# Optimization experiments

Hardware: AMD Instinct MI355X
Metric: run time of the kernel (lower is better)

The kernel has to match this reference:

```python
import jax, jax.numpy as jnp
import numpy as np

M = 0.25
S = 64.0  # gamma
OP = 1.0 + M      # optimum for positives
ON = -M           # optimum for negatives
DELTA_P = 1.0 - M
DELTA_N = M
EPS = 1e-12       # F.normalize eps

B, D, C = 256, 512, 100000


def setup_inputs() -> dict:
    key = jax.random.key(0)
    k1, k2, k3, k4 = jax.random.split(key, 4)
    x = jax.random.normal(k1, (B, D), dtype=jnp.float32)
    emb = jax.random.normal(k2, (B, D), dtype=jnp.float32)
    W = jax.random.normal(k3, (C, D), dtype=jnp.float32) * 0.02  # fc.weight [C, D]
    labels = jax.random.randint(k4, (B,), 0, C, dtype=jnp.int64)
    return {"x": x, "labels": labels, "emb": emb, "W": W}


def reference(x, labels, emb, W):
    # x is unused in the original forward (dead argument)
    # F.normalize(emb): L2-normalize rows with eps clamp
    norm = jnp.linalg.norm(emb, axis=1, keepdims=True)
    ff = emb / jnp.maximum(norm, EPS)
    # fc(ff): linear classifier (weights NOT normalized; the torch loop is a no-op)
    wf = ff @ W.T  # [B, C]
    wf_d = jax.lax.stop_gradient(wf)

    rows = jnp.arange(wf.shape[0])
    sp_logit = wf[rows, labels]        # torch.diagonal(wf.T[labels])
    sp_logit_d = wf_d[rows, labels]

    alpha_p = jnp.maximum(OP - sp_logit_d, 0.0)          # clamp_min(-s_p + Op, 0)
    sp = jnp.exp(-S * alpha_p * (sp_logit - DELTA_P))    # [B]

    # negatives: all classes except the label column (mask instead of cat-slicing)
    neg_mask = jnp.asarray(rows[:, None] >= 0, wf.dtype) * (1.0 - jax.nn.one_hot(labels, wf.shape[1], dtype=wf.dtype))
    alpha_n = jnp.maximum(wf_d + M, 0.0)                 # clamp_min(s_n - On, 0)
    sn = jnp.exp(S * alpha_n * (wf - DELTA_N)) * neg_mask  # label column zeroed out

    loss = jnp.log(1.0 + sn.sum() * sp.sum())
    return loss
```

## Files before the change

### kernel.cpp

```cpp
#include <hip/hip_runtime.h>
#include <hip/hip_bf16.h>

typedef __attribute__((ext_vector_type(8))) __bf16 bf16x8;
typedef __attribute__((ext_vector_type(4))) float f32x4;

#define B_M 256
#define K_D 512
#define N_C 100000
#define BN 64
#define BK 64
#define NBLK ((N_C + BN - 1) / BN)

__device__ __forceinline__ unsigned short f2bf(float x) {
  unsigned int u = __float_as_uint(x);
  u += 0x7fffu + ((u >> 16) & 1u);
  return (unsigned short)(u >> 16);
}

__global__ __launch_bounds__(256) void norm_kernel(const float* __restrict__ emb,
                                                   unsigned short* __restrict__ ff) {
  const int row = blockIdx.x;
  const int t = threadIdx.x;
  float a = emb[row * K_D + t];
  float b = emb[row * K_D + t + 256];
  float ss = a * a + b * b;
  #pragma unroll
  for (int o = 32; o > 0; o >>= 1) ss += __shfl_down(ss, o, 64);
  __shared__ float red[4];
  const int wid = t >> 6, lane = t & 63;
  if (lane == 0) red[wid] = ss;
  __syncthreads();
  float tot = red[0] + red[1] + red[2] + red[3];
  float rn = 1.0f / fmaxf(sqrtf(tot), 1e-12f);
  ff[row * K_D + t]       = f2bf(a * rn);
  ff[row * K_D + t + 256] = f2bf(b * rn);
}

__global__ __launch_bounds__(512) void gemm_loss_kernel(const unsigned short* __restrict__ ff,
                                                        const float* __restrict__ W,
                                                        const int* __restrict__ labels,
                                                        double* __restrict__ partials) {
  __shared__ __align__(16) unsigned short As[B_M * BK];
  __shared__ __align__(16) unsigned short Bs[BN * BK];
  __shared__ int lbl[B_M];
  __shared__ double red[16];

  const int tid = threadIdx.x;
  const int wid = tid >> 6;
  const int lane = tid & 63;
  const int n0 = blockIdx.x * BN;

  if (tid < B_M) lbl[tid] = labels[tid];

  f32x4 acc[2][4] = {};

  const int wrow = wid * 32;
  const int l15 = lane & 15;
  const int lhi = lane >> 4;

  const int bcol = tid >> 3;
  const int bk8  = tid & 7;
  const long long jrow = (long long)n0 + bcol;

  for (int kk = 0; kk < K_D / BK; ++kk) {
    if (kk) __syncthreads();
    #pragma unroll
    for (int it = 0; it < 4; ++it) {
      int idx = it * 512 + tid;
      int row = idx >> 3;
      int kc  = idx & 7;
      uint4 v = *reinterpret_cast<const uint4*>(ff + row * K_D + kk * BK + kc * 8);
      int off = (row * 128 + kc * 16) ^ ((row & 7) << 4);
      *reinterpret_cast<uint4*>(reinterpret_cast<char*>(As) + off) = v;
    }
    {
      float4 f0 = {0.f, 0.f, 0.f, 0.f}, f1 = {0.f, 0.f, 0.f, 0.f};
      if (jrow < N_C) {
        const float* gp = W + jrow * K_D + kk * BK + bk8 * 8;
        f0 = *reinterpret_cast<const float4*>(gp);
        f1 = *reinterpret_cast<const float4*>(gp + 4);
      }
      union { unsigned short us[8]; uint4 v; } pk;
      pk.us[0] = f2bf(f0.x); pk.us[1] = f2bf(f0.y); pk.us[2] = f2bf(f0.z); pk.us[3] = f2bf(f0.w);
      pk.us[4] = f2bf(f1.x); pk.us[5] = f2bf(f1.y); pk.us[6] = f2bf(f1.z); pk.us[7] = f2bf(f1.w);
      int off = (bcol * 128 + bk8 * 16) ^ ((bcol & 7) << 4);
      *reinterpret_cast<uint4*>(reinterpret_cast<char*>(Bs) + off) = pk.v;
    }
    __syncthreads();

    bf16x8 afr[2][2], bfr[4][2];
    #pragma unroll
    for (int fm = 0; fm < 2; ++fm)
      #pragma unroll
      for (int ks = 0; ks < 2; ++ks) {
        int row = wrow + fm * 16 + l15;
        int off = (row * 128 + ks * 64 + lhi * 16) ^ ((row & 7) << 4);
        afr[fm][ks] = *reinterpret_cast<const bf16x8*>(reinterpret_cast<const char*>(As) + off);
      }
    #pragma unroll
    for (int fn = 0; fn < 4; ++fn)
      #pragma unroll
      for (int ks = 0; ks < 2; ++ks) {
        int col = fn * 16 + l15;
        int off = (col * 128 + ks * 64 + lhi * 16) ^ ((col & 7) << 4);
        bfr[fn][ks] = *reinterpret_cast<const bf16x8*>(reinterpret_cast<const char*>(Bs) + off);
      }
    #pragma unroll
    for (int fm = 0; fm < 2; ++fm)
      #pragma unroll
      for (int fn = 0; fn < 4; ++fn)
        #pragma unroll
        for (int ks = 0; ks < 2; ++ks)
          acc[fm][fn] = __builtin_amdgcn_mfma_f32_16x16x32_bf16(afr[fm][ks], bfr[fn][ks], acc[fm][fn], 0, 0, 0);
  }

  float sn_local = 0.0f;
  double sp_local = 0.0;
  #pragma unroll
  for (int fm = 0; fm < 2; ++fm)
    #pragma unroll
    for (int fn = 0; fn < 4; ++fn)
      #pragma unroll
      for (int r = 0; r < 4; ++r) {
        int row = wrow + fm * 16 + lhi * 4 + r;
        int j = n0 + fn * 16 + l15;
        float v = acc[fm][fn][r];
        if (j < N_C) {
          if (j == lbl[row]) {
            double alpha = fmax(1.25 - (double)v, 0.0);
            sp_local += exp(-64.0 * alpha * ((double)v - 0.75));
          } else {
            float an = fmaxf(v + 0.25f, 0.0f);
            sn_local += __expf(64.0f * an * (v - 0.25f));
          }
        }
      }

  double sn_d = (double)sn_local;
  #pragma unroll
  for (int o = 32; o > 0; o >>= 1) {
    sn_d     += __shfl_down(sn_d, o, 64);
    sp_local += __shfl_down(sp_local, o, 64);
  }
  if (lane == 0) { red[wid] = sn_d; red[8 + wid] = sp_local; }
  __syncthreads();
  if (tid == 0) {
    double a = 0.0, b = 0.0;
    #pragma unroll
    for (int i = 0; i < 8; ++i) { a += red[i]; b += red[8 + i]; }
    partials[blockIdx.x] = a;
    partials[NBLK + blockIdx.x] = b;
  }
}

__global__ __launch_bounds__(512) void finalize_kernel(const double* __restrict__ partials,
                                                       float* __restrict__ out) {
  const int t = threadIdx.x;
  double sn = 0.0, sp = 0.0;
  for (int i = t; i < NBLK; i += 512) { sn += partials[i]; sp += partials[NBLK + i]; }
  #pragma unroll
  for (int o = 32; o > 0; o >>= 1) { sn += __shfl_down(sn, o, 64); sp += __shfl_down(sp, o, 64); }
  __shared__ double red[16];
  const int wid = t >> 6, lane = t & 63;
  if (lane == 0) { red[wid] = sn; red[8 + wid] = sp; }
  __syncthreads();
  if (t == 0) {
    double a = 0.0, b = 0.0;
    for (int i = 0; i < 8; ++i) { a += red[i]; b += red[8 + i]; }
    out[0] = (float)log1p(a * b);
  }
}

extern "C" void kernel_launch(void* const* d_in, const int* in_sizes, int n_in,
                              void* d_out, int out_size, void* d_ws, size_t ws_size,
                              hipStream_t stream) {
  const int*   labels = (const int*)d_in[1];
  const float* emb    = (const float*)d_in[2];
  const float* W      = (const float*)d_in[3];
  float* out = (float*)d_out;

  unsigned short* ff = (unsigned short*)d_ws;
  double* partials = (double*)((char*)d_ws + (size_t)B_M * K_D * 2);

  norm_kernel<<<B_M, 256, 0, stream>>>(emb, ff);
  gemm_loss_kernel<<<NBLK, 512, 0, stream>>>(ff, W, labels, partials);
  finalize_kernel<<<1, 512, 0, stream>>>(partials, out);
}
```

Baseline: 73.61 us.

## Pipeline W loads with register prefetch and double-buffered LDS, load A directly

Drops the shared-memory staging of the normalized activations and has each wave load its A fragments straight from global memory, prefetching the next k-step. W tiles are prefetched three steps ahead into registers and written into a double-buffered LDS tile, so there is a single barrier per k-step. This is meant to hide global-load latency behind the MFMA work and cut LDS traffic and barrier count. In exchange it raises register pressure and moves the A traffic onto uncoalesced per-lane global (L2-cached) reads.

```diff
diff --git a/kernel.cpp b/kernel.cpp
--- a/kernel.cpp
+++ b/kernel.cpp
@@ -8,13 +8,20 @@
 #define K_D 512
 #define N_C 100000
 #define BN 64
-#define BK 64
+#define BKS 64
+#define NSTEP (K_D / BKS)
 #define NBLK ((N_C + BN - 1) / BN)
 
 __device__ __forceinline__ unsigned short f2bf(float x) {
   unsigned int u = __float_as_uint(x);
   u += 0x7fffu + ((u >> 16) & 1u);
   return (unsigned short)(u >> 16);
+}
+
+__device__ __forceinline__ void block_sync() {
+  asm volatile("s_waitcnt lgkmcnt(0)" ::: "memory");
+  __builtin_amdgcn_s_barrier();
+  __builtin_amdgcn_sched_barrier(0);
 }
 
 __global__ __launch_bounds__(256) void norm_kernel(const float* __restrict__ emb,
@@ -40,91 +47,105 @@
                                                         const float* __restrict__ W,
                                                         const int* __restrict__ labels,
                                                         double* __restrict__ partials) {
-  __shared__ __align__(16) unsigned short As[B_M * BK];
-  __shared__ __align__(16) unsigned short Bs[BN * BK];
+  __shared__ __align__(16) unsigned short Bs[2][BN * BKS];
   __shared__ int lbl[B_M];
   __shared__ double red[16];
 
   const int tid = threadIdx.x;
   const int wid = tid >> 6;
   const int lane = tid & 63;
-  const int n0 = blockIdx.x * BN;
-
-  if (tid < B_M) lbl[tid] = labels[tid];
-
-  f32x4 acc[2][4] = {};
-
-  const int wrow = wid * 32;
   const int l15 = lane & 15;
   const int lhi = lane >> 4;
+  const int n0 = blockIdx.x * BN;
+
+  if (tid < B_M) lbl[tid] = labels[tid];
 
   const int bcol = tid >> 3;
   const int bk8  = tid & 7;
-  const long long jrow = (long long)n0 + bcol;
-
-  for (int kk = 0; kk < K_D / BK; ++kk) {
-    if (kk) __syncthreads();
-    #pragma unroll
-    for (int it = 0; it < 4; ++it) {
-      int idx = it * 512 + tid;
-      int row = idx >> 3;
-      int kc  = idx & 7;
-      uint4 v = *reinterpret_cast<const uint4*>(ff + row * K_D + kk * BK + kc * 8);
-      int off = (row * 128 + kc * 16) ^ ((row & 7) << 4);
-      *reinterpret_cast<uint4*>(reinterpret_cast<char*>(As) + off) = v;
-    }
-    {
-      float4 f0 = {0.f, 0.f, 0.f, 0.f}, f1 = {0.f, 0.f, 0.f, 0.f};
-      if (jrow < N_C) {
-        const float* gp = W + jrow * K_D + kk * BK + bk8 * 8;
-        f0 = *reinterpret_cast<const float4*>(gp);
-        f1 = *reinterpret_cast<const float4*>(gp + 4);
-      }
-      union { unsigned short us[8]; uint4 v; } pk;
-      pk.us[0] = f2bf(f0.x); pk.us[1] = f2bf(f0.y); pk.us[2] = f2bf(f0.z); pk.us[3] = f2bf(f0.w);
-      pk.us[4] = f2bf(f1.x); pk.us[5] = f2bf(f1.y); pk.us[6] = f2bf(f1.z); pk.us[7] = f2bf(f1.w);
-      int off = (bcol * 128 + bk8 * 16) ^ ((bcol & 7) << 4);
-      *reinterpret_cast<uint4*>(reinterpret_cast<char*>(Bs) + off) = pk.v;
-    }
-    __syncthreads();
-
-    bf16x8 afr[2][2], bfr[4][2];
-    #pragma unroll
-    for (int fm = 0; fm < 2; ++fm)
-      #pragma unroll
-      for (int ks = 0; ks < 2; ++ks) {
-        int row = wrow + fm * 16 + l15;
-        int off = (row * 128 + ks * 64 + lhi * 16) ^ ((row & 7) << 4);
-        afr[fm][ks] = *reinterpret_cast<const bf16x8*>(reinterpret_cast<const char*>(As) + off);
-      }
-    #pragma unroll
-    for (int fn = 0; fn < 4; ++fn)
-      #pragma unroll
-      for (int ks = 0; ks < 2; ++ks) {
-        int col = fn * 16 + l15;
-        int off = (col * 128 + ks * 64 + lhi * 16) ^ ((col & 7) << 4);
-        bfr[fn][ks] = *reinterpret_cast<const bf16x8*>(reinterpret_cast<const char*>(Bs) + off);
-      }
-    #pragma unroll
-    for (int fm = 0; fm < 2; ++fm)
-      #pragma unroll
-      for (int fn = 0; fn < 4; ++fn)
+  const bool valid = (n0 + bcol) < N_C;
+  const float* wp = W + (long long)(n0 + bcol) * K_D + bk8 * 8;
+  const int woff = (bcol * 128 + bk8 * 16) ^ ((bcol & 7) << 4);
+
+  const unsigned short* ap = ff + (wid * 32 + l15) * K_D + lhi * 8;
+
+  f32x4 acc[2][4] = {};
+  float4 wf0[3], wf1[3];
+  bf16x8 acur[2][2], anxt[2][2];
+
+  #pragma unroll
+  for (int mt = 0; mt < 2; ++mt)
+    #pragma unroll
+    for (int ks = 0; ks < 2; ++ks)
+      acur[mt][ks] = *reinterpret_cast<const bf16x8*>(ap + mt * 16 * K_D + ks * 32);
+
+  #pragma unroll
+  for (int s = 0; s < 3; ++s) {
+    if (valid) {
+      wf0[s] = *reinterpret_cast<const float4*>(wp + s * BKS);
+      wf1[s] = *reinterpret_cast<const float4*>(wp + s * BKS + 4);
+    } else {
+      wf0[s] = float4{0.f, 0.f, 0.f, 0.f};
+      wf1[s] = float4{0.f, 0.f, 0.f, 0.f};
+    }
+  }
+  {
+    union { unsigned short us[8]; uint4 v; } pk;
+    pk.us[0] = f2bf(wf0[0].x); pk.us[1] = f2bf(wf0[0].y); pk.us[2] = f2bf(wf0[0].z); pk.us[3] = f2bf(wf0[0].w);
+    pk.us[4] = f2bf(wf1[0].x); pk.us[5] = f2bf(wf1[0].y); pk.us[6] = f2bf(wf1[0].z); pk.us[7] = f2bf(wf1[0].w);
+    *reinterpret_cast<uint4*>(reinterpret_cast<char*>(&Bs[0][0]) + woff) = pk.v;
+  }
+  block_sync();
+
+  #pragma unroll
+  for (int t = 0; t < NSTEP; ++t) {
+    const int cb = t & 1;
+    if (t + 3 < NSTEP && valid) {
+      wf0[t % 3] = *reinterpret_cast<const float4*>(wp + (t + 3) * BKS);
+      wf1[t % 3] = *reinterpret_cast<const float4*>(wp + (t + 3) * BKS + 4);
+    }
+    if (t + 1 < NSTEP) {
+      #pragma unroll
+      for (int mt = 0; mt < 2; ++mt)
         #pragma unroll
         for (int ks = 0; ks < 2; ++ks)
-          acc[fm][fn] = __builtin_amdgcn_mfma_f32_16x16x32_bf16(afr[fm][ks], bfr[fn][ks], acc[fm][fn], 0, 0, 0);
+          anxt[mt][ks] = *reinterpret_cast<const bf16x8*>(ap + mt * 16 * K_D + (t + 1) * BKS + ks * 32);
+      const int s = (t + 1) % 3;
+      union { unsigned short us[8]; uint4 v; } pk;
+      pk.us[0] = f2bf(wf0[s].x); pk.us[1] = f2bf(wf0[s].y); pk.us[2] = f2bf(wf0[s].z); pk.us[3] = f2bf(wf0[s].w);
+      pk.us[4] = f2bf(wf1[s].x); pk.us[5] = f2bf(wf1[s].y); pk.us[6] = f2bf(wf1[s].z); pk.us[7] = f2bf(wf1[s].w);
+      *reinterpret_cast<uint4*>(reinterpret_cast<char*>(&Bs[cb ^ 1][0]) + woff) = pk.v;
+    }
+    #pragma unroll
+    for (int fn = 0; fn < 4; ++fn) {
+      #pragma unroll
+      for (int ks = 0; ks < 2; ++ks) {
+        const int col = fn * 16 + l15;
+        const int boff = (col * 128 + ks * 64 + lhi * 16) ^ ((col & 7) << 4);
+        bf16x8 b = *reinterpret_cast<const bf16x8*>(reinterpret_cast<const char*>(&Bs[cb][0]) + boff);
+        #pragma unroll
+        for (int mt = 0; mt < 2; ++mt)
+          acc[mt][fn] = __builtin_amdgcn_mfma_f32_16x16x32_bf16(acur[mt][ks], b, acc[mt][fn], 0, 0, 0);
+      }
+    }
+    block_sync();
+    #pragma unroll
+    for (int mt = 0; mt < 2; ++mt)
+      #pragma unroll
+      for (int ks = 0; ks < 2; ++ks)
+        acur[mt][ks] = anxt[mt][ks];
   }
 
   float sn_local = 0.0f;
   double sp_local = 0.0;
   #pragma unroll
-  for (int fm = 0; fm < 2; ++fm)
+  for (int mt = 0; mt < 2; ++mt)
     #pragma unroll
     for (int fn = 0; fn < 4; ++fn)
       #pragma unroll
       for (int r = 0; r < 4; ++r) {
-        int row = wrow + fm * 16 + lhi * 4 + r;
+        int row = wid * 32 + mt * 16 + lhi * 4 + r;
         int j = n0 + fn * 16 + l15;
-        float v = acc[fm][fn][r];
+        float v = acc[mt][fn][r];
         if (j < N_C) {
           if (j == lbl[row]) {
             double alpha = fmax(1.25 - (double)v, 0.0);
```

Result: slower. 80.93 us (+10.0%).

## Double-buffer ff tile via direct global-to-LDS loads and register-prefetch W fragments

Applied to the files above, without the earlier changes.

Restructures the GEMM main loop. The ff tile is double-buffered in LDS using global_load_lds with an XOR swizzle. W is no longer staged through LDS: each wave reads its 16 W columns straight into registers, prefetched two K-steps ahead, and converts them to bf16 in place. The warp layout changes to 2x4 so each wave computes 128 rows by 16 columns. The goal is to overlap global loads with MFMA work and remove the W shared-memory round trip, at the cost of hand-written waitcnt and sched_barrier sequencing that is fragile and adds register pressure.

```diff
diff --git a/kernel.cpp b/kernel.cpp
--- a/kernel.cpp
+++ b/kernel.cpp
@@ -9,12 +9,28 @@
 #define N_C 100000
 #define BN 64
 #define BK 64
+#define NSTEP (K_D / BK)
 #define NBLK ((N_C + BN - 1) / BN)
+
+#define SB() __builtin_amdgcn_sched_barrier(0)
 
 __device__ __forceinline__ unsigned short f2bf(float x) {
   unsigned int u = __float_as_uint(x);
   u += 0x7fffu + ((u >> 16) & 1u);
   return (unsigned short)(u >> 16);
+}
+
+__device__ __forceinline__ bf16x8 pack8(float4 a, float4 b) {
+  union { unsigned short us[8]; bf16x8 v; } u;
+  u.us[0] = f2bf(a.x); u.us[1] = f2bf(a.y); u.us[2] = f2bf(a.z); u.us[3] = f2bf(a.w);
+  u.us[4] = f2bf(b.x); u.us[5] = f2bf(b.y); u.us[6] = f2bf(b.z); u.us[7] = f2bf(b.w);
+  return u.v;
+}
+
+__device__ __forceinline__ void glds16(const void* g, void* l) {
+  __builtin_amdgcn_global_load_lds(
+      (const __attribute__((address_space(1))) unsigned int*)g,
+      (__attribute__((address_space(3))) unsigned int*)l, 16, 0, 0);
 }
 
 __global__ __launch_bounds__(256) void norm_kernel(const float* __restrict__ emb,
@@ -40,101 +56,118 @@
                                                         const float* __restrict__ W,
                                                         const int* __restrict__ labels,
                                                         double* __restrict__ partials) {
-  __shared__ __align__(16) unsigned short As[B_M * BK];
-  __shared__ __align__(16) unsigned short Bs[BN * BK];
+  __shared__ __align__(16) unsigned short As[2][B_M * BK];
   __shared__ int lbl[B_M];
   __shared__ double red[16];
 
   const int tid = threadIdx.x;
   const int wid = tid >> 6;
   const int lane = tid & 63;
-  const int n0 = blockIdx.x * BN;
-
-  if (tid < B_M) lbl[tid] = labels[tid];
-
-  f32x4 acc[2][4] = {};
-
-  const int wrow = wid * 32;
   const int l15 = lane & 15;
   const int lhi = lane >> 4;
-
-  const int bcol = tid >> 3;
-  const int bk8  = tid & 7;
-  const long long jrow = (long long)n0 + bcol;
-
-  for (int kk = 0; kk < K_D / BK; ++kk) {
-    if (kk) __syncthreads();
-    #pragma unroll
-    for (int it = 0; it < 4; ++it) {
-      int idx = it * 512 + tid;
-      int row = idx >> 3;
-      int kc  = idx & 7;
-      uint4 v = *reinterpret_cast<const uint4*>(ff + row * K_D + kk * BK + kc * 8);
-      int off = (row * 128 + kc * 16) ^ ((row & 7) << 4);
-      *reinterpret_cast<uint4*>(reinterpret_cast<char*>(As) + off) = v;
-    }
+  const int wm = wid & 1;
+  const int wn = wid >> 1;
+  const int n0 = blockIdx.x * BN;
+
+  if (tid < B_M) lbl[tid] = labels[tid];
+  SB();
+
+  const int jreal = n0 + wn * 16 + l15;
+  const int jcol = jreal < N_C ? jreal : (N_C - 1);
+  const float* wp = W + (long long)jcol * K_D + lhi * 8;
+
+  const int ao0 = l15 * 128 + ((0 * 64 + lhi * 16) ^ ((l15 & 7) << 4));
+  const int ao1 = l15 * 128 + ((1 * 64 + lhi * 16) ^ ((l15 & 7) << 4));
+
+  f32x4 acc[8] = {};
+  float4 wbuf[2][4];
+  bf16x8 bfr[2];
+
+  #pragma unroll
+  for (int it = 0; it < 4; ++it) {
+    int s = it * 512 + tid;
+    int row = s >> 3;
+    int k8 = (s & 7) ^ (row & 7);
+    glds16(ff + row * K_D + 0 * BK + k8 * 8, &As[0][0] + s * 8);
+  }
+  SB();
+  #pragma unroll
+  for (int st = 0; st < 2; ++st) {
+    wbuf[st][0] = *reinterpret_cast<const float4*>(wp + st * BK);
+    wbuf[st][1] = *reinterpret_cast<const float4*>(wp + st * BK + 4);
+    wbuf[st][2] = *reinterpret_cast<const float4*>(wp + st * BK + 32);
+    wbuf[st][3] = *reinterpret_cast<const float4*>(wp + st * BK + 36);
+  }
+  SB();
+  asm volatile("s_waitcnt vmcnt(8)" ::: "memory");
+  asm volatile("s_waitcnt lgkmcnt(0)" ::: "memory");
+  __builtin_amdgcn_s_barrier();
+  SB();
+
+  #pragma unroll
+  for (int t = 0; t < NSTEP; ++t) {
+    if (t + 1 < NSTEP) {
+      #pragma unroll
+      for (int it = 0; it < 4; ++it) {
+        int s = it * 512 + tid;
+        int row = s >> 3;
+        int k8 = (s & 7) ^ (row & 7);
+        glds16(ff + row * K_D + (t + 1) * BK + k8 * 8, &As[(t + 1) & 1][0] + s * 8);
+      }
+    }
+    SB();
+    if (t == 0) {
+      bfr[0] = pack8(wbuf[0][0], wbuf[0][1]);
+      bfr[1] = pack8(wbuf[0][2], wbuf[0][3]);
+      SB();
+    }
+    if (t + 2 < NSTEP) {
+      wbuf[t & 1][0] = *reinterpret_cast<const float4*>(wp + (t + 2) * BK);
+      wbuf[t & 1][1] = *reinterpret_cast<const float4*>(wp + (t + 2) * BK + 4);
+      wbuf[t & 1][2] = *reinterpret_cast<const float4*>(wp + (t + 2) * BK + 32);
+      wbuf[t & 1][3] = *reinterpret_cast<const float4*>(wp + (t + 2) * BK + 36);
+    }
+    SB();
     {
-      float4 f0 = {0.f, 0.f, 0.f, 0.f}, f1 = {0.f, 0.f, 0.f, 0.f};
-      if (jrow < N_C) {
-        const float* gp = W + jrow * K_D + kk * BK + bk8 * 8;
-        f0 = *reinterpret_cast<const float4*>(gp);
-        f1 = *reinterpret_cast<const float4*>(gp + 4);
+      const char* ab = reinterpret_cast<const char*>(&As[t & 1][0]);
+      #pragma unroll
+      for (int mf = 0; mf < 8; ++mf) {
+        const int base = (wm * 8 + mf) * 2048;
+        bf16x8 a0 = *reinterpret_cast<const bf16x8*>(ab + base + ao0);
+        bf16x8 a1 = *reinterpret_cast<const bf16x8*>(ab + base + ao1);
+        acc[mf] = __builtin_amdgcn_mfma_f32_16x16x32_bf16(a0, bfr[0], acc[mf], 0, 0, 0);
+        acc[mf] = __builtin_amdgcn_mfma_f32_16x16x32_bf16(a1, bfr[1], acc[mf], 0, 0, 0);
       }
-      union { unsigned short us[8]; uint4 v; } pk;
-      pk.us[0] = f2bf(f0.x); pk.us[1] = f2bf(f0.y); pk.us[2] = f2bf(f0.z); pk.us[3] = f2bf(f0.w);
-      pk.us[4] = f2bf(f1.x); pk.us[5] = f2bf(f1.y); pk.us[6] = f2bf(f1.z); pk.us[7] = f2bf(f1.w);
-      int off = (bcol * 128 + bk8 * 16) ^ ((bcol & 7) << 4);
-      *reinterpret_cast<uint4*>(reinterpret_cast<char*>(Bs) + off) = pk.v;
-    }
-    __syncthreads();
-
-    bf16x8 afr[2][2], bfr[4][2];
-    #pragma unroll
-    for (int fm = 0; fm < 2; ++fm)
-      #pragma unroll
-      for (int ks = 0; ks < 2; ++ks) {
-        int row = wrow + fm * 16 + l15;
-        int off = (row * 128 + ks * 64 + lhi * 16) ^ ((row & 7) << 4);
-        afr[fm][ks] = *reinterpret_cast<const bf16x8*>(reinterpret_cast<const char*>(As) + off);
-      }
-    #pragma unroll
-    for (int fn = 0; fn < 4; ++fn)
-      #pragma unroll
-      for (int ks = 0; ks < 2; ++ks) {
-        int col = fn * 16 + l15;
-        int off = (col * 128 + ks * 64 + lhi * 16) ^ ((col & 7) << 4);
-        bfr[fn][ks] = *reinterpret_cast<const bf16x8*>(reinterpret_cast<const char*>(Bs) + off);
-      }
-    #pragma unroll
-    for (int fm = 0; fm < 2; ++fm)
-      #pragma unroll
-      for (int fn = 0; fn < 4; ++fn)
-        #pragma unroll
-        for (int ks = 0; ks < 2; ++ks)
-          acc[fm][fn] = __builtin_amdgcn_mfma_f32_16x16x32_bf16(afr[fm][ks], bfr[fn][ks], acc[fm][fn], 0, 0, 0);
+    }
+    if (t + 1 < NSTEP) {
+      if (t + 2 < NSTEP) { asm volatile("s_waitcnt vmcnt(4)" ::: "memory"); }
+      else               { asm volatile("s_waitcnt vmcnt(0)" ::: "memory"); }
+      bfr[0] = pack8(wbuf[(t + 1) & 1][0], wbuf[(t + 1) & 1][1]);
+      bfr[1] = pack8(wbuf[(t + 1) & 1][2], wbuf[(t + 1) & 1][3]);
+      asm volatile("s_waitcnt lgkmcnt(0)" ::: "memory");
+      __builtin_amdgcn_s_barrier();
+      SB();
+    }
   }
 
   float sn_local = 0.0f;
   double sp_local = 0.0;
-  #pragma unroll
-  for (int fm = 0; fm < 2; ++fm)
+  if (jreal < N_C) {
     #pragma unroll
-    for (int fn = 0; fn < 4; ++fn)
+    for (int mf = 0; mf < 8; ++mf)
       #pragma unroll
       for (int r = 0; r < 4; ++r) {
-        int row = wrow + fm * 16 + lhi * 4 + r;
-        int j = n0 + fn * 16 + l15;
-        float v = acc[fm][fn][r];
-        if (j < N_C) {
-          if (j == lbl[row]) {
-            double alpha = fmax(1.25 - (double)v, 0.0);
-            sp_local += exp(-64.0 * alpha * ((double)v - 0.75));
-          } else {
-            float an = fmaxf(v + 0.25f, 0.0f);
-            sn_local += __expf(64.0f * an * (v - 0.25f));
-          }
+        int row = wm * 128 + mf * 16 + lhi * 4 + r;
+        float v = acc[mf][r];
+        if (jreal == lbl[row]) {
+          double alpha = fmax(1.25 - (double)v, 0.0);
+          sp_local += exp(-64.0 * alpha * ((double)v - 0.75));
+        } else {
+          float an = fmaxf(v + 0.25f, 0.0f);
+          sn_local += __expf(64.0f * an * (v - 0.25f));
         }
       }
+  }
 
   double sn_d = (double)sn_local;
   #pragma unroll
```

Measured after the change: 92.58 us. 25.8% more time.

## Replace LDS-staged GEMM with per-wave 64x64 register tiles loaded from global

Applied to the files above, without the earlier changes.

The shared-memory staging of A and B tiles and its barriers are removed. Each wave now computes an independent 64x64 output tile, loading bf16 A fragments and f32 W fragments directly from global memory into MFMA registers. This removes LDS traffic and synchronization. In exchange, each W tile is fetched and converted by four waves instead of once, and the global loads are strided per lane rather than coalesced.

```diff
diff --git a/kernel.cpp b/kernel.cpp
--- a/kernel.cpp
+++ b/kernel.cpp
@@ -7,14 +7,23 @@
 #define B_M 256
 #define K_D 512
 #define N_C 100000
-#define BN 64
-#define BK 64
-#define NBLK ((N_C + BN - 1) / BN)
+#define TM 64
+#define TN 64
+#define NT_N ((N_C + TN - 1) / TN)
+#define N_TILES (4 * NT_N)
+#define NBLK2 ((N_TILES + 7) / 8)
 
 __device__ __forceinline__ unsigned short f2bf(float x) {
   unsigned int u = __float_as_uint(x);
   u += 0x7fffu + ((u >> 16) & 1u);
   return (unsigned short)(u >> 16);
+}
+
+__device__ __forceinline__ bf16x8 pack8(float4 a, float4 b) {
+  union { unsigned short us[8]; bf16x8 v; } u;
+  u.us[0] = f2bf(a.x); u.us[1] = f2bf(a.y); u.us[2] = f2bf(a.z); u.us[3] = f2bf(a.w);
+  u.us[4] = f2bf(b.x); u.us[5] = f2bf(b.y); u.us[6] = f2bf(b.z); u.us[7] = f2bf(b.w);
+  return u.v;
 }
 
 __global__ __launch_bounds__(256) void norm_kernel(const float* __restrict__ emb,
@@ -40,93 +49,73 @@
                                                         const float* __restrict__ W,
                                                         const int* __restrict__ labels,
                                                         double* __restrict__ partials) {
-  __shared__ __align__(16) unsigned short As[B_M * BK];
-  __shared__ __align__(16) unsigned short Bs[BN * BK];
   __shared__ int lbl[B_M];
   __shared__ double red[16];
 
   const int tid = threadIdx.x;
   const int wid = tid >> 6;
   const int lane = tid & 63;
-  const int n0 = blockIdx.x * BN;
-
-  if (tid < B_M) lbl[tid] = labels[tid];
-
-  f32x4 acc[2][4] = {};
-
-  const int wrow = wid * 32;
   const int l15 = lane & 15;
   const int lhi = lane >> 4;
 
-  const int bcol = tid >> 3;
-  const int bk8  = tid & 7;
-  const long long jrow = (long long)n0 + bcol;
+  if (tid < B_M) lbl[tid] = labels[tid];
+  __syncthreads();
 
-  for (int kk = 0; kk < K_D / BK; ++kk) {
-    if (kk) __syncthreads();
+  const int tile = blockIdx.x * 8 + wid;
+  const bool live = tile < N_TILES;
+  const int mt = (tile & 3) * TM;
+  const int nt = (tile >> 2) * TN;
+
+  const unsigned short* apf[4];
+  const float* wpf[4];
+  bool cvalid[4];
+  #pragma unroll
+  for (int i = 0; i < 4; ++i) {
+    int arow = mt + i * 16 + l15;
+    apf[i] = ff + arow * K_D + lhi * 8;
+    int col = nt + i * 16 + l15;
+    cvalid[i] = live && (col < N_C);
+    int cc = (col < N_C && live) ? col : 0;
+    wpf[i] = W + (long long)cc * K_D + lhi * 8;
+  }
+
+  f32x4 acc[4][4] = {};
+
+  if (live) {
     #pragma unroll
-    for (int it = 0; it < 4; ++it) {
-      int idx = it * 512 + tid;
-      int row = idx >> 3;
-      int kc  = idx & 7;
-      uint4 v = *reinterpret_cast<const uint4*>(ff + row * K_D + kk * BK + kc * 8);
-      int off = (row * 128 + kc * 16) ^ ((row & 7) << 4);
-      *reinterpret_cast<uint4*>(reinterpret_cast<char*>(As) + off) = v;
+    for (int kk = 0; kk < 16; ++kk) {
+      bf16x8 afr[4], bfr[4];
+      #pragma unroll
+      for (int i = 0; i < 4; ++i)
+        afr[i] = *reinterpret_cast<const bf16x8*>(apf[i] + kk * 32);
+      #pragma unroll
+      for (int i = 0; i < 4; ++i) {
+        float4 lo = *reinterpret_cast<const float4*>(wpf[i] + kk * 32);
+        float4 hi = *reinterpret_cast<const float4*>(wpf[i] + kk * 32 + 4);
+        bfr[i] = pack8(lo, hi);
+      }
+      #pragma unroll
+      for (int am = 0; am < 4; ++am)
+        #pragma unroll
+        for (int bn = 0; bn < 4; ++bn)
+          acc[am][bn] = __builtin_amdgcn_mfma_f32_16x16x32_bf16(afr[am], bfr[bn], acc[am][bn], 0, 0, 0);
     }
-    {
-      float4 f0 = {0.f, 0.f, 0.f, 0.f}, f1 = {0.f, 0.f, 0.f, 0.f};
-      if (jrow < N_C) {
-        const float* gp = W + jrow * K_D + kk * BK + bk8 * 8;
-        f0 = *reinterpret_cast<const float4*>(gp);
-        f1 = *reinterpret_cast<const float4*>(gp + 4);
-      }
-      union { unsigned short us[8]; uint4 v; } pk;
-      pk.us[0] = f2bf(f0.x); pk.us[1] = f2bf(f0.y); pk.us[2] = f2bf(f0.z); pk.us[3] = f2bf(f0.w);
-      pk.us[4] = f2bf(f1.x); pk.us[5] = f2bf(f1.y); pk.us[6] = f2bf(f1.z); pk.us[7] = f2bf(f1.w);
-      int off = (bcol * 128 + bk8 * 16) ^ ((bcol & 7) << 4);
-      *reinterpret_cast<uint4*>(reinterpret_cast<char*>(Bs) + off) = pk.v;
-    }
-    __syncthreads();
-
-    bf16x8 afr[2][2], bfr[4][2];
-    #pragma unroll
-    for (int fm = 0; fm < 2; ++fm)
-      #pragma unroll
-      for (int ks = 0; ks < 2; ++ks) {
-        int row = wrow + fm * 16 + l15;
-        int off = (row * 128 + ks * 64 + lhi * 16) ^ ((row & 7) << 4);
-        afr[fm][ks] = *reinterpret_cast<const bf16x8*>(reinterpret_cast<const char*>(As) + off);
-      }
-    #pragma unroll
-    for (int fn = 0; fn < 4; ++fn)
-      #pragma unroll
-      for (int ks = 0; ks < 2; ++ks) {
-        int col = fn * 16 + l15;
-        int off = (col * 128 + ks * 64 + lhi * 16) ^ ((col & 7) << 4);
-        bfr[fn][ks] = *reinterpret_cast<const bf16x8*>(reinterpret_cast<const char*>(Bs) + off);
-      }
-    #pragma unroll
-    for (int fm = 0; fm < 2; ++fm)
-      #pragma unroll
-      for (int fn = 0; fn < 4; ++fn)
-        #pragma unroll
-        for (int ks = 0; ks < 2; ++ks)
-          acc[fm][fn] = __builtin_amdgcn_mfma_f32_16x16x32_bf16(afr[fm][ks], bfr[fn][ks], acc[fm][fn], 0, 0, 0);
   }
 
   float sn_local = 0.0f;
   double sp_local = 0.0;
   #pragma unroll
-  for (int fm = 0; fm < 2; ++fm)
+  for (int bn = 0; bn < 4; ++bn) {
+    const int col = nt + bn * 16 + l15;
+    const bool cv = cvalid[bn];
     #pragma unroll
-    for (int fn = 0; fn < 4; ++fn)
+    for (int am = 0; am < 4; ++am)
       #pragma unroll
       for (int r = 0; r < 4; ++r) {
-        int row = wrow + fm * 16 + lhi * 4 + r;
-        int j = n0 + fn * 16 + l15;
-        float v = acc[fm][fn][r];
-        if (j < N_C) {
-          if (j == lbl[row]) {
+        const int row = mt + am * 16 + lhi * 4 + r;
+        float v = acc[am][bn][r];
+        if (cv) {
+          if (col == lbl[row]) {
             double alpha = fmax(1.25 - (double)v, 0.0);
             sp_local += exp(-64.0 * alpha * ((double)v - 0.75));
           } else {
@@ -135,6 +124,7 @@
           }
         }
       }
+  }
 
   double sn_d = (double)sn_local;
   #pragma unroll
@@ -149,7 +139,7 @@
     #pragma unroll
     for (int i = 0; i < 8; ++i) { a += red[i]; b += red[8 + i]; }
     partials[blockIdx.x] = a;
-    partials[NBLK + blockIdx.x] = b;
+    partials[NBLK2 + blockIdx.x] = b;
   }
 }
 
@@ -157,7 +147,7 @@
                                                        float* __restrict__ out) {
   const int t = threadIdx.x;
   double sn = 0.0, sp = 0.0;
-  for (int i = t; i < NBLK; i += 512) { sn += partials[i]; sp += partials[NBLK + i]; }
+  for (int i = t; i < NBLK2; i += 512) { sn += partials[i]; sp += partials[NBLK2 + i]; }
   #pragma unroll
   for (int o = 32; o > 0; o >>= 1) { sn += __shfl_down(sn, o, 64); sp += __shfl_down(sp, o, 64); }
   __shared__ double red[16];
@@ -183,6 +173,6 @@
   double* partials = (double*)((char*)d_ws + (size_t)B_M * K_D * 2);
 
   norm_kernel<<<B_M, 256, 0, stream>>>(emb, ff);
-  gemm_loss_kernel<<<NBLK, 512, 0, stream>>>(ff, W, labels, partials);
+  gemm_loss_kernel<<<NBLK2, 512, 0, stream>>>(ff, W, labels, partials);
   finalize_kernel<<<1, 512, 0, stream>>>(partials, out);
 }
```

New measurement: 205.9 us. +179.7%, slower.
